# Kernel tuning notes

Measured on AMD Instinct MI355X. Metric: run time of the kernel, lower is better.

## Reference

```python
import jax, jax.numpy as jnp
import numpy as np

N_EMBD = 2560
N_HEAD = 32
HEAD_DIM = N_EMBD // N_HEAD  # 80
ROTARY_DIM = 32
SEQ = 2048
BSZ = 1


def _rope_tables(seq_len, rotary_dim, base=10000.0):
    inv_freq = 1.0 / (base ** (np.arange(0, rotary_dim, 2, dtype=np.float32) / rotary_dim))
    t = np.arange(seq_len, dtype=np.float32)
    freqs = np.outer(t, inv_freq)                      # [S, rd/2]
    emb = np.concatenate([freqs, freqs], axis=-1)      # [S, rd]
    return jnp.asarray(np.cos(emb)), jnp.asarray(np.sin(emb))


def setup_inputs() -> dict:
    key = jax.random.key(0)
    k1, k2, k3, k4, k5 = jax.random.split(key, 5)
    op_size = HEAD_DIM * (N_HEAD + 2 * N_HEAD)  # fused q,k,v => 3*n_embd
    hidden_states = jax.random.normal(k1, (BSZ, SEQ, N_EMBD), dtype=jnp.float32)
    Wqkv_w = jax.random.normal(k2, (op_size, N_EMBD), dtype=jnp.float32) * 0.02
    Wqkv_b = jax.random.normal(k3, (op_size,), dtype=jnp.float32) * 0.02
    out_w = jax.random.normal(k4, (N_EMBD, N_EMBD), dtype=jnp.float32) * 0.02
    out_b = jax.random.normal(k5, (N_EMBD,), dtype=jnp.float32) * 0.02
    cos, sin = _rope_tables(SEQ, ROTARY_DIM)
    return {"hidden_states": hidden_states, "Wqkv_w": Wqkv_w, "Wqkv_b": Wqkv_b,
            "out_w": out_w, "out_b": out_b, "cos": cos, "sin": sin}


def apply_partial_rotary(x, cos, sin):
    # x: [S, B, H, D]; cos/sin: [S, rd]
    rd = cos.shape[-1]
    c = cos[:, None, None, :]
    s = sin[:, None, None, :]
    x_rot = x[..., :rd]
    # NOTE: faithful to source -- rotated half is concatenated WITHOUT negation
    tmp = jnp.concatenate([x[..., rd // 2:rd], x[..., :rd // 2]], axis=-1)
    rotten = x_rot * c + tmp * s
    return jnp.concatenate([rotten, x[..., rd:]], axis=-1)


def reference(hidden_states, Wqkv_w, Wqkv_b, out_w, out_b, cos, sin):
    bsz, q_len, _ = hidden_states.shape
    qkv = hidden_states @ Wqkv_w.T + Wqkv_b            # [B, S, 3*E]
    q, k, v = jnp.split(qkv, 3, axis=-1)
    # [B, S, H, D] -> [S, B, H, D] for rotary
    q = q.reshape(bsz, q_len, N_HEAD, HEAD_DIM).transpose(1, 0, 2, 3)
    k = k.reshape(bsz, q_len, N_HEAD, HEAD_DIM).transpose(1, 0, 2, 3)
    v = v.reshape(bsz, q_len, N_HEAD, HEAD_DIM).transpose(0, 2, 1, 3)  # [B, H, S, D]
    cos_t, sin_t = cos[:q_len], sin[:q_len]
    q = apply_partial_rotary(q, cos_t, sin_t).transpose(1, 2, 0, 3)    # [B, H, S, D]
    k = apply_partial_rotary(k, cos_t, sin_t).transpose(1, 2, 0, 3)    # [B, H, S, D]
    scale = 1.0 / jnp.sqrt(jnp.asarray(HEAD_DIM, dtype=q.dtype))
    scores = jnp.einsum('bhqd,bhkd->bhqk', q, k) * scale
    causal = jnp.tril(jnp.ones((q_len, q_len), dtype=bool))
    scores = jnp.where(causal, scores, jnp.asarray(-1e30, dtype=scores.dtype))
    probs = jax.nn.softmax(scores, axis=-1)
    out = jnp.einsum('bhqk,bhkd->bhqd', probs, v)       # [B, H, S, D]
    out = out.transpose(0, 2, 1, 3).reshape(bsz, q_len, N_EMBD)
    return out @ out_w.T + out_b
```

## Files before the change

kernel.cpp:

```cpp
#include <hip/hip_runtime.h>
#include <cstdint>
#include <cstddef>

typedef unsigned short bf16_t;
typedef __attribute__((ext_vector_type(8))) short bf16x8;
typedef __attribute__((ext_vector_type(4))) float f32x4;

__device__ __forceinline__ float bf2f(bf16_t b) {
  unsigned int u = ((unsigned int)b) << 16;
  return __builtin_bit_cast(float, u);
}
__device__ __forceinline__ bf16_t f2bf(float f) {
  unsigned int u = __builtin_bit_cast(unsigned int, f);
  u += 0x7fffu + ((u >> 16) & 1u);
  return (bf16_t)(u >> 16);
}
__device__ __forceinline__ float exp2_hw(float x) {
  return __builtin_amdgcn_exp2f(x);
}

constexpr int SEQ = 2048, NE = 2560, NH = 32, HD = 80, OP = 7680;

__global__ void cvt3(const float* __restrict__ s0, const float* __restrict__ s1,
                     const float* __restrict__ s2, bf16_t* __restrict__ d0,
                     bf16_t* __restrict__ d1, bf16_t* __restrict__ d2)
{
  constexpr int N0 = SEQ * NE / 4, N1 = OP * NE / 4;
  int t = blockIdx.x * 256 + threadIdx.x;
  const float* s; bf16_t* d;
  if (t < N0)            { s = s0; d = d0; }
  else if (t < N0 + N1)  { s = s1; d = d1; t -= N0; }
  else                   { s = s2; d = d2; t -= N0 + N1; }
  float4 v = ((const float4*)s)[t];
  ushort4 o;
  o.x = f2bf(v.x); o.y = f2bf(v.y); o.z = f2bf(v.z); o.w = f2bf(v.w);
  ((ushort4*)d)[t] = o;
}

__device__ __forceinline__ void store_out(bf16_t* p, float v) { *p = f2bf(v); }
__device__ __forceinline__ void store_out(float* p, float v)  { *p = v; }

__global__ __launch_bounds__(512, 2) void gemm256_bt_bias(
    const bf16_t* __restrict__ A,
    const bf16_t* __restrict__ B,
    const float*  __restrict__ bias,
    bf16_t* __restrict__ C,
    int M, int N, int K)
{
  __shared__ bf16_t As[2][256 * 64];
  __shared__ bf16_t Bs[2][256 * 64];

  const int tid  = threadIdx.x;
  const int lane = tid & 63;
  const int wave = tid >> 6;
  const int wm   = wave >> 2;
  const int wn   = wave & 3;
  const int lm   = lane & 15;
  const int quad = lane >> 4;
  const int m0 = blockIdx.y * 256;
  const int n0 = blockIdx.x * 256;
  const int NT = K / 64;

  const int srow = lane >> 3;
  const int scol = ((lane & 7) ^ srow) * 8;

  auto stage = [&](const bf16_t* __restrict__ P, int R0, int K0, int H, bf16_t* DST) {
#pragma unroll
    for (int cc = 0; cc < 2; ++cc) {
      const int seg = wave * 2 + cc;
      const bf16_t* src = P + (size_t)(R0 + H * 128 + seg * 8 + srow) * K + K0 + scol;
      __builtin_amdgcn_global_load_lds(
          (const __attribute__((address_space(1))) unsigned int*)src,
          (__attribute__((address_space(3))) unsigned int*)(DST + H * 8192 + seg * 512),
          16, 0, 0);
    }
  };

  const int xk0 = ((0 + quad) ^ (lm & 7)) * 8;
  const int xk1 = ((4 + quad) ^ (lm & 7)) * 8;

  const int AOFF = (wm * 128 + lm) * 64;
  const int BOFF = (wn * 64  + lm) * 64;

  f32x4 acc[8][4];
#pragma unroll
  for (int i = 0; i < 8; ++i)
#pragma unroll
    for (int j = 0; j < 4; ++j)
      acc[i][j] = (f32x4){0.f, 0.f, 0.f, 0.f};

  stage(A, m0, 0, 0, As[0]);  stage(A, m0, 0, 1, As[0]);
  stage(B, n0, 0, 0, Bs[0]);  stage(B, n0, 0, 1, Bs[0]);
  stage(A, m0, 64, 0, As[1]); stage(A, m0, 64, 1, As[1]);
  stage(B, n0, 64, 0, Bs[1]); stage(B, n0, 64, 1, Bs[1]);

  asm volatile("s_waitcnt vmcnt(8)" ::: "memory");
  __builtin_amdgcn_s_barrier();
  __builtin_amdgcn_sched_barrier(0);

  bf16x8 a[4][2], b01[2][2], b23[2][2];
#pragma unroll
  for (int j = 0; j < 2; ++j) {
    b01[j][0] = *(const bf16x8*)(&Bs[0][BOFF + j * 1024 + xk0]);
    b01[j][1] = *(const bf16x8*)(&Bs[0][BOFF + j * 1024 + xk1]);
  }
#pragma unroll
  for (int i = 0; i < 4; ++i) {
    a[i][0] = *(const bf16x8*)(&As[0][AOFF + i * 1024 + xk0]);
    a[i][1] = *(const bf16x8*)(&As[0][AOFF + i * 1024 + xk1]);
  }
  __builtin_amdgcn_sched_barrier(0);

  for (int t = 0; t < NT; ++t) {
    const int c = t & 1;
    const bf16_t* Ac = &As[c][0];
    const bf16_t* Bc = &Bs[c][0];
    const bf16_t* An = &As[c ^ 1][0];
    const bf16_t* Bn = &Bs[c ^ 1][0];

    __builtin_amdgcn_s_setprio(1);
#pragma unroll
    for (int kk = 0; kk < 2; ++kk)
#pragma unroll
      for (int i = 0; i < 2; ++i)
#pragma unroll
        for (int j = 0; j < 2; ++j)
          acc[i][j] = __builtin_amdgcn_mfma_f32_16x16x32_bf16(a[i][kk], b01[j][kk], acc[i][j], 0, 0, 0);
    __builtin_amdgcn_s_setprio(0);
#pragma unroll
    for (int j = 0; j < 2; ++j) {
      b23[j][0] = *(const bf16x8*)(Bc + BOFF + (2 + j) * 1024 + xk0);
      b23[j][1] = *(const bf16x8*)(Bc + BOFF + (2 + j) * 1024 + xk1);
    }
    __builtin_amdgcn_sched_barrier(0);
    __builtin_amdgcn_s_setprio(1);
#pragma unroll
    for (int kk = 0; kk < 2; ++kk)
#pragma unroll
      for (int i = 2; i < 4; ++i)
#pragma unroll
        for (int j = 0; j < 2; ++j)
          acc[i][j] = __builtin_amdgcn_mfma_f32_16x16x32_bf16(a[i][kk], b01[j][kk], acc[i][j], 0, 0, 0);
    __builtin_amdgcn_s_setprio(0);
    __builtin_amdgcn_sched_barrier(0);

    __builtin_amdgcn_s_setprio(1);
#pragma unroll
    for (int kk = 0; kk < 2; ++kk)
#pragma unroll
      for (int i = 0; i < 4; ++i)
#pragma unroll
        for (int j = 0; j < 2; ++j)
          acc[i][2 + j] = __builtin_amdgcn_mfma_f32_16x16x32_bf16(a[i][kk], b23[j][kk], acc[i][2 + j], 0, 0, 0);
    __builtin_amdgcn_s_setprio(0);
#pragma unroll
    for (int i = 0; i < 4; ++i) {
      a[i][0] = *(const bf16x8*)(Ac + AOFF + 4096 + i * 1024 + xk0);
      a[i][1] = *(const bf16x8*)(Ac + AOFF + 4096 + i * 1024 + xk1);
    }
    __builtin_amdgcn_sched_barrier(0);

    __builtin_amdgcn_s_setprio(1);
#pragma unroll
    for (int kk = 0; kk < 2; ++kk)
#pragma unroll
      for (int i = 0; i < 4; ++i)
#pragma unroll
        for (int j = 0; j < 2; ++j)
          acc[4 + i][j] = __builtin_amdgcn_mfma_f32_16x16x32_bf16(a[i][kk], b01[j][kk], acc[4 + i][j], 0, 0, 0);
    __builtin_amdgcn_s_setprio(0);
    __builtin_amdgcn_sched_barrier(0);

    asm volatile("s_waitcnt lgkmcnt(0)" ::: "memory");
    asm volatile("s_waitcnt vmcnt(0)"  ::: "memory");
    __builtin_amdgcn_s_barrier();
    __builtin_amdgcn_sched_barrier(0);
    if (t + 1 < NT) {
#pragma unroll
      for (int j = 0; j < 2; ++j) {
        b01[j][0] = *(const bf16x8*)(Bn + BOFF + j * 1024 + xk0);
        b01[j][1] = *(const bf16x8*)(Bn + BOFF + j * 1024 + xk1);
      }
    }
    __builtin_amdgcn_sched_barrier(0);

    __builtin_amdgcn_s_setprio(1);
#pragma unroll
    for (int kk = 0; kk < 2; ++kk)
#pragma unroll
      for (int i = 0; i < 4; ++i)
#pragma unroll
        for (int j = 0; j < 2; ++j)
          acc[4 + i][2 + j] = __builtin_amdgcn_mfma_f32_16x16x32_bf16(a[i][kk], b23[j][kk], acc[4 + i][2 + j], 0, 0, 0);
    __builtin_amdgcn_s_setprio(0);
    if (t + 2 < NT) {
      stage(B, n0, (t + 2) * 64, 0, (bf16_t*)Bs[c]);
      stage(B, n0, (t + 2) * 64, 1, (bf16_t*)Bs[c]);
      stage(A, m0, (t + 2) * 64, 0, (bf16_t*)As[c]);
      stage(A, m0, (t + 2) * 64, 1, (bf16_t*)As[c]);
    }
    if (t + 1 < NT) {
#pragma unroll
      for (int i = 0; i < 4; ++i) {
        a[i][0] = *(const bf16x8*)(An + AOFF + i * 1024 + xk0);
        a[i][1] = *(const bf16x8*)(An + AOFF + i * 1024 + xk1);
      }
    }
    __builtin_amdgcn_sched_barrier(0);
  }

#pragma unroll
  for (int i = 0; i < 8; ++i) {
#pragma unroll
    for (int j = 0; j < 4; ++j) {
      const int n = n0 + wn * 64 + j * 16 + lm;
      const float bv = bias ? bias[n] : 0.f;
#pragma unroll
      for (int r = 0; r < 4; ++r) {
        const int m = m0 + wm * 128 + i * 16 + quad * 4 + r;
        C[(size_t)m * N + n] = f2bf(acc[i][j][r] + bv);
      }
    }
  }
}

template <typename OutT>
__global__ __launch_bounds__(256, 2) void gemm_bt_bias(
    const bf16_t* __restrict__ A,
    const bf16_t* __restrict__ B,
    const float*  __restrict__ bias,
    OutT* __restrict__ C,
    int M, int N, int K, int klen)
{
  __shared__ bf16_t As[2][128 * 32];
  __shared__ bf16_t Bs[2][128 * 32];

  const int tid  = threadIdx.x;
  const int lane = tid & 63;
  const int wave = tid >> 6;
  const int m0 = blockIdx.y * 128;
  const int n0 = blockIdx.x * 128;
  const int kbeg = blockIdx.z * klen;
  OutT* Cz = C + (size_t)blockIdx.z * M * N;
  const int mw = (wave >> 1) * 64;
  const int nw = (wave & 1) * 64;
  const int lm = lane & 15;
  const int lq = lane >> 4;

  f32x4 acc[4][4];
#pragma unroll
  for (int i = 0; i < 4; ++i)
#pragma unroll
    for (int j = 0; j < 4; ++j)
      acc[i][j] = (f32x4){0.f, 0.f, 0.f, 0.f};

  const int ldr = lane >> 2;
  const int ldc = (lane & 3) * 8;

  for (int kt = kbeg; kt < kbeg + klen; kt += 64) {
#pragma unroll
    for (int sub = 0; sub < 2; ++sub) {
#pragma unroll
      for (int r = 0; r < 2; ++r) {
        const int seg = wave * 2 + r;
        const int row = seg * 16 + ldr;
        const int col = kt + sub * 32 + ldc;
        const bf16_t* ga = A + (size_t)(m0 + row) * K + col;
        const bf16_t* gb = B + (size_t)(n0 + row) * K + col;
        __builtin_amdgcn_global_load_lds(
            (const __attribute__((address_space(1))) unsigned int*)ga,
            (__attribute__((address_space(3))) unsigned int*)&As[sub][seg * 512], 16, 0, 0);
        __builtin_amdgcn_global_load_lds(
            (const __attribute__((address_space(1))) unsigned int*)gb,
            (__attribute__((address_space(3))) unsigned int*)&Bs[sub][seg * 512], 16, 0, 0);
      }
    }
    __syncthreads();

#pragma unroll
    for (int sub = 0; sub < 2; ++sub) {
      bf16x8 af[4], bfq[4];
#pragma unroll
      for (int i = 0; i < 4; ++i)
        af[i] = *(const bf16x8*)&As[sub][(mw + i * 16 + lm) * 32 + lq * 8];
#pragma unroll
      for (int j = 0; j < 4; ++j)
        bfq[j] = *(const bf16x8*)&Bs[sub][(nw + j * 16 + lm) * 32 + lq * 8];

#pragma unroll
      for (int i = 0; i < 4; ++i)
#pragma unroll
        for (int j = 0; j < 4; ++j)
          acc[i][j] = __builtin_amdgcn_mfma_f32_16x16x32_bf16(af[i], bfq[j], acc[i][j], 0, 0, 0);
    }

    __syncthreads();
  }

#pragma unroll
  for (int i = 0; i < 4; ++i) {
#pragma unroll
    for (int j = 0; j < 4; ++j) {
      const int n = n0 + nw + j * 16 + lm;
      const float bv = bias ? bias[n] : 0.f;
#pragma unroll
      for (int r = 0; r < 4; ++r) {
        const int m = m0 + mw + i * 16 + lq * 4 + r;
        store_out(&Cz[(size_t)m * N + n], acc[i][j][r] + bv);
      }
    }
  }
}

__global__ void reduce2_bias(const float* __restrict__ p, const float* __restrict__ bias,
                             float* __restrict__ out)
{
  const int t = blockIdx.x * 256 + threadIdx.x;
  const float4 a = ((const float4*)p)[t];
  const float4 b = ((const float4*)(p + (size_t)SEQ * NE))[t];
  const float4 bv = ((const float4*)bias)[t % (NE / 4)];
  float4 r;
  r.x = a.x + b.x + bv.x; r.y = a.y + b.y + bv.y;
  r.z = a.z + b.z + bv.z; r.w = a.w + b.w + bv.w;
  ((float4*)out)[t] = r;
}

constexpr int TSTR = 82;
__global__ void rope_vtrans(bf16_t* __restrict__ qkv,
                            const float* __restrict__ cosb,
                            const float* __restrict__ sinb,
                            bf16_t* __restrict__ vtg)
{
  __shared__ bf16_t T[64 * TSTR];
  const int tid = threadIdx.x;

  if (blockIdx.x < 8192) {
    const int t = blockIdx.x * 256 + tid;
    const int i  = t & 15;
    const int qk = (t >> 4) & 1;
    const int h  = (t >> 5) & 31;
    const int s  = t >> 10;
    const size_t base = (size_t)s * OP + qk * NE + h * HD;
    const float xi = bf2f(qkv[base + i]);
    const float xj = bf2f(qkv[base + i + 16]);
    const float c1 = cosb[s * 32 + i];
    const float s1 = sinb[s * 32 + i];
    const float c2 = cosb[s * 32 + i + 16];
    const float s2 = sinb[s * 32 + i + 16];
    qkv[base + i]      = f2bf(xi * c1 + xj * s1);
    qkv[base + i + 16] = f2bf(xj * c2 + xi * s2);
    return;
  }

  const int vb = blockIdx.x - 8192;
  const int h  = vb >> 5;
  const int sb = (vb & 31) * 64;
  const int voff = 2 * NE + h * HD;

#pragma unroll
  for (int i = 0; i < 10; ++i) {
    const int u = i * 256 + tid;
    const int row = u / 40, c = u % 40;
    const unsigned int w = *(const unsigned int*)(qkv + (size_t)(sb + row) * OP + voff + 2 * c);
    *(unsigned int*)&T[row * TSTR + 2 * c] = w;
  }
  __syncthreads();

  bf16_t* vh = vtg + (size_t)h * HD * SEQ;
#pragma unroll
  for (int i = 0; i < 10; ++i) {
    const int u = i * 256 + tid;
    const int d = u >> 5, sp = u & 31;
    const unsigned int lo = T[(2 * sp) * TSTR + d];
    const unsigned int hi = T[(2 * sp + 1) * TSTR + d];
    *(unsigned int*)(vh + (size_t)d * SEQ + sb + 2 * sp) = lo | (hi << 16);
  }
}

constexpr int KSTR = 104;
constexpr int VSTR = 72;
constexpr int PSTR = 72;

__global__ __launch_bounds__(256, 4) void attn_mfma(
    const bf16_t* __restrict__ qkv, const bf16_t* __restrict__ vtg,
    bf16_t* __restrict__ aout)
{
  __shared__ bf16_t Ks[64 * KSTR];
  __shared__ bf16_t Vt[12 * 512];
  __shared__ bf16_t Ps[4][16 * PSTR];

  const int z  = blockIdx.x;
  const int s4 = z >> 8;
  const int h  = z & 31;
  const int g  = (z >> 5) & 7;
  const int qt = (s4 == 0) ? g : (s4 == 1) ? 15 - g : (s4 == 2) ? 16 + g : 31 - g;
  const int q0 = qt * 64;
  const int tid  = threadIdx.x;
  const int lane = tid & 63;
  const int wave = tid >> 6;
  const int lm   = lane & 15;
  const int quad = lane >> 4;

  const int qg = q0 + 16 * wave + lm;

  const int koff = NE + h * HD;
  const bf16_t* vh = vtg + (size_t)h * HD * SEQ;
  const float EC = 0.1118033988749895f * 1.4426950408889634f;

  bf16x8 qf[3];
  {
    const bf16_t* q_r = qkv + (size_t)qg * OP + h * HD;
#pragma unroll
    for (int ks = 0; ks < 3; ++ks) {
      const int col = ks * 32 + quad * 8;
      if (col < 80) qf[ks] = *(const bf16x8*)(q_r + col);
      else          qf[ks] = (bf16x8){0,0,0,0,0,0,0,0};
    }
  }

  int kofs[4];
#pragma unroll
  for (int r = 0; r < 4; ++r) {
    const int seg = (r < 3) ? wave * 3 + r : 12;
    const int e = seg * 512 + lane * 8;
    const int row = e / KSTR, c = e % KSTR;
    kofs[r] = row * OP + (c < 80 ? c : c - 24);
  }
  int vofs[3];
#pragma unroll
  for (int r = 0; r < 3; ++r) {
    const int e = (wave * 3 + r) * 512 + lane * 8;
    int row = e / 72;
    const int c = e % 72;
    if (row >= 80) row -= 80;
    vofs[r] = row * SEQ + (c < 64 ? c : c - 16);
  }

  f32x4 oacc[5];
#pragma unroll
  for (int mt = 0; mt < 5; ++mt) oacc[mt] = (f32x4){0.f,0.f,0.f,0.f};
  float lsum = 0.f;

  const int ntiles = qt + 1;
  for (int t = 0; t < ntiles; ++t) {
    const int kb = t * 64;

#pragma unroll
    for (int r = 0; r < 3; ++r) {
      const bf16_t* gk = qkv + (size_t)kb * OP + koff + kofs[r];
      __builtin_amdgcn_global_load_lds(
          (const __attribute__((address_space(1))) unsigned int*)gk,
          (__attribute__((address_space(3))) unsigned int*)&Ks[(wave * 3 + r) * 512],
          16, 0, 0);
      const bf16_t* gv = vh + kb + vofs[r];
      __builtin_amdgcn_global_load_lds(
          (const __attribute__((address_space(1))) unsigned int*)gv,
          (__attribute__((address_space(3))) unsigned int*)&Vt[(wave * 3 + r) * 512],
          16, 0, 0);
    }
    if (wave == 3) {
      const bf16_t* gk = qkv + (size_t)kb * OP + koff + kofs[3];
      __builtin_amdgcn_global_load_lds(
          (const __attribute__((address_space(1))) unsigned int*)gk,
          (__attribute__((address_space(3))) unsigned int*)&Ks[12 * 512],
          16, 0, 0);
    }
    __syncthreads();

    f32x4 sacc[4];
#pragma unroll
    for (int mt = 0; mt < 4; ++mt) sacc[mt] = (f32x4){0.f,0.f,0.f,0.f};
#pragma unroll
    for (int ks = 0; ks < 3; ++ks) {
      bf16x8 kf[4];
#pragma unroll
      for (int mt = 0; mt < 4; ++mt)
        kf[mt] = *(const bf16x8*)&Ks[(mt * 16 + lm) * KSTR + ks * 32 + quad * 8];
#pragma unroll
      for (int mt = 0; mt < 4; ++mt)
        sacc[mt] = __builtin_amdgcn_mfma_f32_16x16x32_bf16(kf[mt], qf[ks], sacc[mt], 0, 0, 0);
    }

    if (t == ntiles - 1) {
      const int keyb = kb + quad * 4;
#pragma unroll
      for (int mt = 0; mt < 4; ++mt) {
        float ps[4];
#pragma unroll
        for (int r = 0; r < 4; ++r) {
          float p = exp2_hw(sacc[mt][r] * EC);
          p = (keyb + mt * 16 + r > qg) ? 0.f : p;
          ps[r] = p;
        }
        lsum += (ps[0] + ps[1]) + (ps[2] + ps[3]);
        ushort4 pk;
        pk.x = f2bf(ps[0]); pk.y = f2bf(ps[1]); pk.z = f2bf(ps[2]); pk.w = f2bf(ps[3]);
        *(ushort4*)&Ps[wave][lm * PSTR + mt * 16 + quad * 4] = pk;
      }
    } else {
#pragma unroll
      for (int mt = 0; mt < 4; ++mt) {
        float ps[4];
#pragma unroll
        for (int r = 0; r < 4; ++r) ps[r] = exp2_hw(sacc[mt][r] * EC);
        lsum += (ps[0] + ps[1]) + (ps[2] + ps[3]);
        ushort4 pk;
        pk.x = f2bf(ps[0]); pk.y = f2bf(ps[1]); pk.z = f2bf(ps[2]); pk.w = f2bf(ps[3]);
        *(ushort4*)&Ps[wave][lm * PSTR + mt * 16 + quad * 4] = pk;
      }
    }

#pragma unroll
    for (int ks = 0; ks < 2; ++ks) {
      bf16x8 vf[5], pf;
#pragma unroll
      for (int mt = 0; mt < 5; ++mt)
        vf[mt] = *(const bf16x8*)&Vt[(mt * 16 + lm) * VSTR + ks * 32 + quad * 8];
      pf = *(const bf16x8*)&Ps[wave][lm * PSTR + ks * 32 + quad * 8];
#pragma unroll
      for (int mt = 0; mt < 5; ++mt)
        oacc[mt] = __builtin_amdgcn_mfma_f32_16x16x32_bf16(vf[mt], pf, oacc[mt], 0, 0, 0);
    }
    __syncthreads();
  }

  lsum += __shfl_xor(lsum, 16);
  lsum += __shfl_xor(lsum, 32);
  const float inv = 1.f / lsum;
  bf16_t* base = aout + (size_t)qg * NE + h * HD + quad * 4;
#pragma unroll
  for (int mt = 0; mt < 5; ++mt) {
    ushort4 st;
    st.x = f2bf(oacc[mt][0] * inv);
    st.y = f2bf(oacc[mt][1] * inv);
    st.z = f2bf(oacc[mt][2] * inv);
    st.w = f2bf(oacc[mt][3] * inv);
    *(ushort4*)(base + mt * 16) = st;
  }
}

extern "C" void kernel_launch(void* const* d_in, const int* in_sizes, int n_in,
                              void* d_out, int out_size, void* d_ws, size_t ws_size,
                              hipStream_t stream)
{
  const float* hs   = (const float*)d_in[0];
  const float* wqkv = (const float*)d_in[1];
  const float* bqkv = (const float*)d_in[2];
  const float* wout = (const float*)d_in[3];
  const float* bout = (const float*)d_in[4];
  const float* cosb = (const float*)d_in[5];
  const float* sinb = (const float*)d_in[6];

  bf16_t* hs_bf   = (bf16_t*)d_ws;
  bf16_t* wqkv_bf = hs_bf   + (size_t)SEQ * NE;
  bf16_t* wout_bf = wqkv_bf + (size_t)OP * NE;
  bf16_t* qkv     = wout_bf + (size_t)NE * NE;
  bf16_t* aout    = qkv     + (size_t)SEQ * OP;
  float*  out     = (float*)d_out;
  bf16_t* vtg     = hs_bf;
  float*  pbuf    = (float*)d_ws;

  constexpr int CVT_T = (SEQ * NE + OP * NE + NE * NE) / 4;
  cvt3<<<CVT_T / 256, 256, 0, stream>>>(hs, wqkv, wout, hs_bf, wqkv_bf, wout_bf);

  gemm256_bt_bias<<<dim3(OP / 256, SEQ / 256), 512, 0, stream>>>(
      hs_bf, wqkv_bf, bqkv, qkv, SEQ, OP, NE);
  rope_vtrans<<<8192 + 1024, 256, 0, stream>>>(qkv, cosb, sinb, vtg);
  attn_mfma<<<1024, 256, 0, stream>>>(qkv, vtg, aout);
  gemm_bt_bias<float><<<dim3(NE / 128, SEQ / 128, 2), 256, 0, stream>>>(
      aout, wout_bf, nullptr, pbuf, SEQ, NE, NE, NE / 2);
  reduce2_bias<<<(SEQ * NE / 4) / 256, 256, 0, stream>>>(pbuf, bout, out);
}
```

Before: 359.2 us.

## Double-buffer K/V tiles in attention and pair causal query tiles per block

The attention kernel now prefetches the next K/V tile into a second LDS buffer while computing on the current one, using async global-to-LDS loads. This hides load latency behind the MFMA work. Each block also processes two query tiles (qt and 31-qt) in sequence, so causal work is balanced and only 512 blocks are launched. The price is doubled LDS use and launch bounds lowered to 2 blocks per CU, which reduces occupancy. Fewer blocks could also leave some CUs underused.

```diff
diff --git a/kernel.cpp b/kernel.cpp
--- a/kernel.cpp
+++ b/kernel.cpp
@@ -381,42 +381,26 @@
 constexpr int VSTR = 72;
 constexpr int PSTR = 72;
 
-__global__ __launch_bounds__(256, 4) void attn_mfma(
+__global__ __launch_bounds__(256, 2) void attn_mfma(
     const bf16_t* __restrict__ qkv, const bf16_t* __restrict__ vtg,
     bf16_t* __restrict__ aout)
 {
-  __shared__ bf16_t Ks[64 * KSTR];
-  __shared__ bf16_t Vt[12 * 512];
+  __shared__ bf16_t Ks[2][13 * 512];
+  __shared__ bf16_t Vt[2][12 * 512];
   __shared__ bf16_t Ps[4][16 * PSTR];
 
-  const int z  = blockIdx.x;
-  const int s4 = z >> 8;
-  const int h  = z & 31;
-  const int g  = (z >> 5) & 7;
-  const int qt = (s4 == 0) ? g : (s4 == 1) ? 15 - g : (s4 == 2) ? 16 + g : 31 - g;
-  const int q0 = qt * 64;
+  const int id = blockIdx.x;
+  const int h  = id & 31;
+  const int uu = id >> 5;
   const int tid  = threadIdx.x;
   const int lane = tid & 63;
   const int wave = tid >> 6;
   const int lm   = lane & 15;
   const int quad = lane >> 4;
 
-  const int qg = q0 + 16 * wave + lm;
-
   const int koff = NE + h * HD;
   const bf16_t* vh = vtg + (size_t)h * HD * SEQ;
   const float EC = 0.1118033988749895f * 1.4426950408889634f;
-
-  bf16x8 qf[3];
-  {
-    const bf16_t* q_r = qkv + (size_t)qg * OP + h * HD;
-#pragma unroll
-    for (int ks = 0; ks < 3; ++ks) {
-      const int col = ks * 32 + quad * 8;
-      if (col < 80) qf[ks] = *(const bf16x8*)(q_r + col);
-      else          qf[ks] = (bf16x8){0,0,0,0,0,0,0,0};
-    }
-  }
 
   int kofs[4];
 #pragma unroll
@@ -436,106 +420,136 @@
     vofs[r] = row * SEQ + (c < 64 ? c : c - 16);
   }
 
-  f32x4 oacc[5];
-#pragma unroll
-  for (int mt = 0; mt < 5; ++mt) oacc[mt] = (f32x4){0.f,0.f,0.f,0.f};
-  float lsum = 0.f;
-
-  const int ntiles = qt + 1;
-  for (int t = 0; t < ntiles; ++t) {
-    const int kb = t * 64;
-
+  auto stage_tile = [&](int kb, int bsel) {
 #pragma unroll
     for (int r = 0; r < 3; ++r) {
       const bf16_t* gk = qkv + (size_t)kb * OP + koff + kofs[r];
       __builtin_amdgcn_global_load_lds(
           (const __attribute__((address_space(1))) unsigned int*)gk,
-          (__attribute__((address_space(3))) unsigned int*)&Ks[(wave * 3 + r) * 512],
+          (__attribute__((address_space(3))) unsigned int*)&Ks[bsel][(wave * 3 + r) * 512],
           16, 0, 0);
       const bf16_t* gv = vh + kb + vofs[r];
       __builtin_amdgcn_global_load_lds(
           (const __attribute__((address_space(1))) unsigned int*)gv,
-          (__attribute__((address_space(3))) unsigned int*)&Vt[(wave * 3 + r) * 512],
+          (__attribute__((address_space(3))) unsigned int*)&Vt[bsel][(wave * 3 + r) * 512],
           16, 0, 0);
     }
     if (wave == 3) {
       const bf16_t* gk = qkv + (size_t)kb * OP + koff + kofs[3];
       __builtin_amdgcn_global_load_lds(
           (const __attribute__((address_space(1))) unsigned int*)gk,
-          (__attribute__((address_space(3))) unsigned int*)&Ks[12 * 512],
+          (__attribute__((address_space(3))) unsigned int*)&Ks[bsel][12 * 512],
           16, 0, 0);
     }
+  };
+
+#pragma unroll 1
+  for (int pass = 0; pass < 2; ++pass) {
+    const int qt = pass ? 31 - uu : uu;
+    const int q0 = qt * 64;
+    const int qg = q0 + 16 * wave + lm;
+
+    bf16x8 qf[3];
+    {
+      const bf16_t* q_r = qkv + (size_t)qg * OP + h * HD;
+#pragma unroll
+      for (int ks = 0; ks < 3; ++ks) {
+        const int col = ks * 32 + quad * 8;
+        if (col < 80) qf[ks] = *(const bf16x8*)(q_r + col);
+        else          qf[ks] = (bf16x8){0,0,0,0,0,0,0,0};
+      }
+    }
+
+    f32x4 oacc[5];
+#pragma unroll
+    for (int mt = 0; mt < 5; ++mt) oacc[mt] = (f32x4){0.f,0.f,0.f,0.f};
+    float lsum = 0.f;
+
+    const int ntiles = qt + 1;
+    stage_tile(0, 0);
     __syncthreads();
 
-    f32x4 sacc[4];
-#pragma unroll
-    for (int mt = 0; mt < 4; ++mt) sacc[mt] = (f32x4){0.f,0.f,0.f,0.f};
-#pragma unroll
-    for (int ks = 0; ks < 3; ++ks) {
-      bf16x8 kf[4];
-#pragma unroll
-      for (int mt = 0; mt < 4; ++mt)
-        kf[mt] = *(const bf16x8*)&Ks[(mt * 16 + lm) * KSTR + ks * 32 + quad * 8];
-#pragma unroll
-      for (int mt = 0; mt < 4; ++mt)
-        sacc[mt] = __builtin_amdgcn_mfma_f32_16x16x32_bf16(kf[mt], qf[ks], sacc[mt], 0, 0, 0);
-    }
-
-    if (t == ntiles - 1) {
-      const int keyb = kb + quad * 4;
-#pragma unroll
-      for (int mt = 0; mt < 4; ++mt) {
-        float ps[4];
-#pragma unroll
-        for (int r = 0; r < 4; ++r) {
-          float p = exp2_hw(sacc[mt][r] * EC);
-          p = (keyb + mt * 16 + r > qg) ? 0.f : p;
-          ps[r] = p;
+    int buf = 0;
+#pragma unroll 1
+    for (int t = 0; t < ntiles; ++t) {
+      if (t + 1 < ntiles) stage_tile((t + 1) * 64, buf ^ 1);
+
+      const bf16_t* Kb = &Ks[buf][0];
+      const bf16_t* Vb = &Vt[buf][0];
+
+      f32x4 sacc[4];
+#pragma unroll
+      for (int mt = 0; mt < 4; ++mt) sacc[mt] = (f32x4){0.f,0.f,0.f,0.f};
+#pragma unroll
+      for (int ks = 0; ks < 3; ++ks) {
+        bf16x8 kf[4];
+#pragma unroll
+        for (int mt = 0; mt < 4; ++mt)
+          kf[mt] = *(const bf16x8*)&Kb[(mt * 16 + lm) * KSTR + ks * 32 + quad * 8];
+#pragma unroll
+        for (int mt = 0; mt < 4; ++mt)
+          sacc[mt] = __builtin_amdgcn_mfma_f32_16x16x32_bf16(kf[mt], qf[ks], sacc[mt], 0, 0, 0);
+      }
+
+      const int kb = t * 64;
+      if (t == ntiles - 1) {
+        const int keyb = kb + quad * 4;
+#pragma unroll
+        for (int mt = 0; mt < 4; ++mt) {
+          float ps[4];
+#pragma unroll
+          for (int r = 0; r < 4; ++r) {
+            float p = exp2_hw(sacc[mt][r] * EC);
+            p = (keyb + mt * 16 + r > qg) ? 0.f : p;
+            ps[r] = p;
+          }
+          lsum += (ps[0] + ps[1]) + (ps[2] + ps[3]);
+          ushort4 pk;
+          pk.x = f2bf(ps[0]); pk.y = f2bf(ps[1]); pk.z = f2bf(ps[2]); pk.w = f2bf(ps[3]);
+          *(ushort4*)&Ps[wave][lm * PSTR + mt * 16 + quad * 4] = pk;
         }
-        lsum += (ps[0] + ps[1]) + (ps[2] + ps[3]);
-        ushort4 pk;
-        pk.x = f2bf(ps[0]); pk.y = f2bf(ps[1]); pk.z = f2bf(ps[2]); pk.w = f2bf(ps[3]);
-        *(ushort4*)&Ps[wave][lm * PSTR + mt * 16 + quad * 4] = pk;
-      }
-    } else {
-#pragma unroll
-      for (int mt = 0; mt < 4; ++mt) {
-        float ps[4];
-#pragma unroll
-        for (int r = 0; r < 4; ++r) ps[r] = exp2_hw(sacc[mt][r] * EC);
-        lsum += (ps[0] + ps[1]) + (ps[2] + ps[3]);
-        ushort4 pk;
-        pk.x = f2bf(ps[0]); pk.y = f2bf(ps[1]); pk.z = f2bf(ps[2]); pk.w = f2bf(ps[3]);
-        *(ushort4*)&Ps[wave][lm * PSTR + mt * 16 + quad * 4] = pk;
-      }
-    }
-
-#pragma unroll
-    for (int ks = 0; ks < 2; ++ks) {
-      bf16x8 vf[5], pf;
-#pragma unroll
-      for (int mt = 0; mt < 5; ++mt)
-        vf[mt] = *(const bf16x8*)&Vt[(mt * 16 + lm) * VSTR + ks * 32 + quad * 8];
-      pf = *(const bf16x8*)&Ps[wave][lm * PSTR + ks * 32 + quad * 8];
-#pragma unroll
-      for (int mt = 0; mt < 5; ++mt)
-        oacc[mt] = __builtin_amdgcn_mfma_f32_16x16x32_bf16(vf[mt], pf, oacc[mt], 0, 0, 0);
-    }
-    __syncthreads();
-  }
-
-  lsum += __shfl_xor(lsum, 16);
-  lsum += __shfl_xor(lsum, 32);
-  const float inv = 1.f / lsum;
-  bf16_t* base = aout + (size_t)qg * NE + h * HD + quad * 4;
-#pragma unroll
-  for (int mt = 0; mt < 5; ++mt) {
-    ushort4 st;
-    st.x = f2bf(oacc[mt][0] * inv);
-    st.y = f2bf(oacc[mt][1] * inv);
-    st.z = f2bf(oacc[mt][2] * inv);
-    st.w = f2bf(oacc[mt][3] * inv);
-    *(ushort4*)(base + mt * 16) = st;
+      } else {
+#pragma unroll
+        for (int mt = 0; mt < 4; ++mt) {
+          float ps[4];
+#pragma unroll
+          for (int r = 0; r < 4; ++r) ps[r] = exp2_hw(sacc[mt][r] * EC);
+          lsum += (ps[0] + ps[1]) + (ps[2] + ps[3]);
+          ushort4 pk;
+          pk.x = f2bf(ps[0]); pk.y = f2bf(ps[1]); pk.z = f2bf(ps[2]); pk.w = f2bf(ps[3]);
+          *(ushort4*)&Ps[wave][lm * PSTR + mt * 16 + quad * 4] = pk;
+        }
+      }
+
+#pragma unroll
+      for (int ks = 0; ks < 2; ++ks) {
+        bf16x8 vf[5], pf;
+#pragma unroll
+        for (int mt = 0; mt < 5; ++mt)
+          vf[mt] = *(const bf16x8*)&Vb[(mt * 16 + lm) * VSTR + ks * 32 + quad * 8];
+        pf = *(const bf16x8*)&Ps[wave][lm * PSTR + ks * 32 + quad * 8];
+#pragma unroll
+        for (int mt = 0; mt < 5; ++mt)
+          oacc[mt] = __builtin_amdgcn_mfma_f32_16x16x32_bf16(vf[mt], pf, oacc[mt], 0, 0, 0);
+      }
+
+      __syncthreads();
+      buf ^= 1;
+    }
+
+    lsum += __shfl_xor(lsum, 16);
+    lsum += __shfl_xor(lsum, 32);
+    const float inv = 1.f / lsum;
+    bf16_t* base = aout + (size_t)qg * NE + h * HD + quad * 4;
+#pragma unroll
+    for (int mt = 0; mt < 5; ++mt) {
+      ushort4 st;
+      st.x = f2bf(oacc[mt][0] * inv);
+      st.y = f2bf(oacc[mt][1] * inv);
+      st.z = f2bf(oacc[mt][2] * inv);
+      st.w = f2bf(oacc[mt][3] * inv);
+      *(ushort4*)(base + mt * 16) = st;
+    }
   }
 }
 
@@ -566,7 +580,7 @@
   gemm256_bt_bias<<<dim3(OP / 256, SEQ / 256), 512, 0, stream>>>(
       hs_bf, wqkv_bf, bqkv, qkv, SEQ, OP, NE);
   rope_vtrans<<<8192 + 1024, 256, 0, stream>>>(qkv, cosb, sinb, vtg);
-  attn_mfma<<<1024, 256, 0, stream>>>(qkv, vtg, aout);
+  attn_mfma<<<512, 256, 0, stream>>>(qkv, vtg, aout);
   gemm_bt_bias<float><<<dim3(NE / 128, SEQ / 128, 2), 256, 0, stream>>>(
       aout, wout_bf, nullptr, pbuf, SEQ, NE, NE, NE / 2);
   reduce2_bias<<<(SEQ * NE / 4) / 256, 256, 0, stream>>>(pbuf, bout, out);
```

Result: no change. 358.3 us (-0.3%).
